# Kernel optimization log

Measured on AMD Instinct MI355X. Metric: run time of the kernel, lower is better.

Reference implementation:

```python
import jax, jax.numpy as jnp
import numpy as np

N = 50000      # nodes
E = 800000     # edges (avg degree 16)
D_IN = 128     # input_dim
H = 64         # hidden_dim (== output_dim)
L = 3          # num_layers


def setup_inputs() -> dict:
    key = jax.random.key(0)
    ks = jax.random.split(key, 24)
    s = 0.05
    p = lambda k, shape: jax.random.normal(k, shape, dtype=jnp.float32) * s
    inp = {}
    inp["node_features"] = jax.random.normal(ks[0], (N, D_IN), dtype=jnp.float32)
    inp["edge_index"] = jax.random.randint(ks[1], (2, E), 0, N, dtype=jnp.int32)
    # pre_mlp: Linear-ReLU-Linear (setup_LRL_nn with hidden_sizes=[hidden_dim])
    inp["pre_w1"] = p(ks[2], (D_IN, H)); inp["pre_b1"] = jnp.zeros((H,), jnp.float32)
    inp["pre_w2"] = p(ks[3], (H, H));    inp["pre_b2"] = jnp.zeros((H,), jnp.float32)
    # learnable skip gates (initialized to ones as in the module)
    inp["skip"] = jnp.ones((L, L), jnp.float32)
    # SAGEConv layers: lin_l (on mean-aggregated neighbors, with bias) + lin_r (root)
    for i in range(L):
        din = H * (i + 1)
        inp[f"wl{i}"] = p(ks[4 + 3 * i], (din, H))
        inp[f"bl{i}"] = jnp.zeros((H,), jnp.float32)
        inp[f"wr{i}"] = p(ks[5 + 3 * i], (din, H))
    # post_mlp: 256->64, 64->64, 64->256, 256->64
    inp["post_w1"] = p(ks[14], (H * (L + 1), H)); inp["post_b1"] = jnp.zeros((H,), jnp.float32)
    inp["post_w2"] = p(ks[15], (H, H));           inp["post_b2"] = jnp.zeros((H,), jnp.float32)
    inp["post_w3"] = p(ks[16], (H, 256));         inp["post_b3"] = jnp.zeros((256,), jnp.float32)
    inp["post_w4"] = p(ks[17], (256, H));         inp["post_b4"] = jnp.zeros((H,), jnp.float32)
    return inp


def _sage(x, src, dst, inv_deg, wl, bl, wr):
    # PyG SAGEConv (mean aggr): lin_l(mean_{j->i} x_j) + lin_r(x_i)
    agg = jax.ops.segment_sum(x[src], dst, num_segments=N) * inv_deg  # [N, Din]
    return agg @ wl + bl + x @ wr


def reference(node_features, edge_index,
              pre_w1, pre_b1, pre_w2, pre_b2, skip,
              wl0, bl0, wr0, wl1, bl1, wr1, wl2, bl2, wr2,
              post_w1, post_b1, post_w2, post_b2, post_w3, post_b3, post_w4, post_b4):
    src, dst = edge_index[0], edge_index[1]
    deg = jax.ops.segment_sum(jnp.ones((E,), jnp.float32), dst, num_segments=N)
    inv_deg = (1.0 / jnp.maximum(deg, 1.0))[:, None]  # [N,1]

    # pre_mlp
    x = jax.nn.relu(node_features @ pre_w1 + pre_b1) @ pre_w2 + pre_b2  # [N,H]

    layers = [(wl0, bl0, wr0), (wl1, bl1, wr1), (wl2, bl2, wr2)]
    all_emb = [x]
    emb = x
    for i, (wl, bl, wr) in enumerate(layers):
        gates = jax.nn.sigmoid(skip[i, :i + 1])  # [i+1]
        curr = jnp.concatenate([all_emb[j] * gates[j] for j in range(i + 1)], axis=1)  # [N, H*(i+1)]
        h = jax.nn.relu(_sage(curr, src, dst, inv_deg, wl, bl, wr))  # [N,H]  (dropout p=0)
        emb = jnp.concatenate([emb, h], axis=1)
        all_emb.append(h)

    s = jnp.sum(emb, axis=-2)  # sums over all nodes -> [H*(L+1)] (faithful to source)
    h = jax.nn.leaky_relu(s @ post_w1 + post_b1, negative_slope=0.1)
    h = jax.nn.relu(h @ post_w2 + post_b2)
    h = jax.nn.relu(h @ post_w3 + post_b3)
    return h @ post_w4 + post_b4  # [H]
```

## Files before the change

### kernel.cpp

```cpp
#include <hip/hip_runtime.h>
#include <math.h>

#define NN 50000
#define NE 800000
#define NB 196

typedef float v4f __attribute__((ext_vector_type(4)));
typedef _Float16 v8h __attribute__((ext_vector_type(8)));


__global__ __launch_bounds__(256) void k_bhist(const int* __restrict__ dst,
                                               int* __restrict__ gbcnt) {
  __shared__ int lcnt[NB];
  int t = threadIdx.x;
  for (int i = t; i < NB; i += 256) lcnt[i] = 0;
  __syncthreads();
  int eb = blockIdx.x * 4096;
#pragma unroll
  for (int i = 0; i < 16; ++i) {
    int e = eb + i * 256 + t;
    if (e < NE) atomicAdd(&lcnt[dst[e] >> 8], 1);
  }
  __syncthreads();
  for (int i = t; i < NB; i += 256)
    if (lcnt[i]) atomicAdd(&gbcnt[i], lcnt[i]);
}

__global__ __launch_bounds__(256) void k_bscan(const int* __restrict__ gbcnt,
                                               int* __restrict__ boff,
                                               int* __restrict__ gcur,
                                               int* __restrict__ offs) {
  __shared__ int sd[256];
  int t = threadIdx.x;
  int v = (t < NB) ? gbcnt[t] : 0;
  sd[t] = v;
  __syncthreads();
  for (int o = 1; o < 256; o <<= 1) {
    int u = (t >= o) ? sd[t - o] : 0;
    __syncthreads();
    sd[t] += u;
    __syncthreads();
  }
  if (t < NB) { int x = sd[t] - v; boff[t] = x; gcur[t] = x; }
  if (t == NB - 1) boff[NB] = sd[t];
  if (t == 0) offs[NN] = NE;
}

__global__ __launch_bounds__(256) void k_bscatter(const int* __restrict__ src,
                                                  const int* __restrict__ dst,
                                                  int* __restrict__ gcur,
                                                  unsigned* __restrict__ ebuf) {
  __shared__ int cnt[NB];
  __shared__ int base[NB];
  int t = threadIdx.x;
  for (int i = t; i < NB; i += 256) cnt[i] = 0;
  __syncthreads();
  int eb = blockIdx.x * 4096;
  unsigned pk[16];
  int bk[16], lp[16];
#pragma unroll
  for (int i = 0; i < 16; ++i) {
    int e = eb + i * 256 + t;
    if (e < NE) {
      int d = dst[e];
      int b = d >> 8;
      pk[i] = ((unsigned)src[e] << 8) | (unsigned)(d & 255);
      bk[i] = b;
      lp[i] = atomicAdd(&cnt[b], 1);
    }
  }
  __syncthreads();
  for (int i = t; i < NB; i += 256)
    base[i] = cnt[i] ? atomicAdd(&gcur[i], cnt[i]) : 0;
  __syncthreads();
#pragma unroll
  for (int i = 0; i < 16; ++i) {
    int e = eb + i * 256 + t;
    if (e < NE) ebuf[base[bk[i]] + lp[i]] = pk[i];
  }
}

__global__ __launch_bounds__(256) void k_bbuild(const unsigned* __restrict__ ebuf,
                                                const int* __restrict__ boff,
                                                int* __restrict__ offs,
                                                float* __restrict__ invd,
                                                int* __restrict__ csr) {
  __shared__ int dcnt[256];
  __shared__ int cur[256];
  int t = threadIdx.x;
  int b = blockIdx.x;
  int node0 = b << 8;
  int es = boff[b], ee = boff[b + 1];
  dcnt[t] = 0;
  __syncthreads();
  for (int e = es + t; e < ee; e += 256) atomicAdd(&dcnt[ebuf[e] & 255], 1);
  __syncthreads();
  int v = dcnt[t];
  cur[t] = v;
  __syncthreads();
  for (int o = 1; o < 256; o <<= 1) {
    int u = (t >= o) ? cur[t - o] : 0;
    __syncthreads();
    cur[t] += u;
    __syncthreads();
  }
  int excl = cur[t] - v;
  int node = node0 + t;
  if (node < NN) {
    offs[node] = es + excl;
    invd[node] = 1.0f / fmaxf((float)v, 1.0f);
  }
  __syncthreads();
  cur[t] = es + excl;
  __syncthreads();
  for (int e = es + t; e < ee; e += 256) {
    unsigned pk = ebuf[e];
    int p = atomicAdd(&cur[pk & 255], 1);
    csr[p] = (int)(pk >> 8);
  }
}

__global__ __launch_bounds__(256) void k_aggregate(
    const _Float16* __restrict__ feat,
    const int* __restrict__ offs, const int* __restrict__ csr,
    const float* __restrict__ invd,
    _Float16* __restrict__ mean, int n) {
  int node = blockIdx.x * 4 + (threadIdx.x >> 6);
  int lane = threadIdx.x & 63;
  int slot = lane >> 3;
  int cg   = lane & 7;
  if (node >= n) return;
  int s = offs[node], e = offs[node + 1];

  float a[8];
#pragma unroll
  for (int i = 0; i < 8; ++i) a[i] = 0.f;

  if (e > s) {
    int emax = e - 1;
    for (int p0 = s; p0 < e; p0 += 16) {
      int pa = p0 + slot, pb = p0 + 8 + slot;
      int ja = __builtin_nontemporal_load(csr + (pa < emax ? pa : emax));
      int jb = __builtin_nontemporal_load(csr + (pb < emax ? pb : emax));
      v8h va = *(const v8h*)(feat + (size_t)ja * 64 + cg * 8);
      v8h vb = *(const v8h*)(feat + (size_t)jb * 64 + cg * 8);
      if (pa < e) {
#pragma unroll
        for (int i = 0; i < 8; ++i) a[i] += (float)va[i];
      }
      if (pb < e) {
#pragma unroll
        for (int i = 0; i < 8; ++i) a[i] += (float)vb[i];
      }
    }
  }
#pragma unroll
  for (int i = 0; i < 8; ++i) {
    a[i] += __shfl_xor(a[i], 8, 64);
    a[i] += __shfl_xor(a[i], 16, 64);
    a[i] += __shfl_xor(a[i], 32, 64);
  }
  if (lane < 8) {
    float d = invd[node];
    v8h o;
#pragma unroll
    for (int i = 0; i < 8; ++i) o[i] = (_Float16)(a[i] * d);
    *(v8h*)(mean + (size_t)node * 64 + lane * 8) = o;
  }
}

struct LinArgs {
  const void*  a[6];
  const float* w[6];
  int gidx[6];
  int stride[6];
  int isf32[6];
  int nsrc;
  const float* bias;
  const float* skip;
  _Float16* outp;
  float* colsum;
  int n;
  int relu;
};

__global__ __launch_bounds__(256) void k_linear(LinArgs A) {
  __shared__ _Float16 sW[2][2][64 * 72];
  const int t    = threadIdx.x;
  const int lane = t & 63;
  const int wv   = t >> 6;
  const int qd   = lane >> 4;
  const int ln   = lane & 15;
  const int n0   = blockIdx.x * 64;

  v4f acc[4];
#pragma unroll
  for (int ct = 0; ct < 4; ++ct) acc[ct] = (v4f){0.f, 0.f, 0.f, 0.f};

  const int sn = t & 63;
  float wreg[16];
  auto loadW = [&](int s) {
    const float* w = A.w[s];
#pragma unroll
    for (int c = 0; c < 2; ++c) {
      int kb = (wv + 4 * c) * 8;
#pragma unroll
      for (int j = 0; j < 8; ++j)
        wreg[c * 8 + j] = w[(size_t)(kb + j) * 64 + sn];
    }
  };
  auto writeW = [&](int s, int b) {
    float gs = 1.0f;
    if (A.gidx[s] >= 0) gs = 1.0f / (1.0f + __expf(-A.skip[A.gidx[s]]));
#pragma unroll
    for (int c = 0; c < 2; ++c) {
      int cb = wv + 4 * c;
      v8h hv, lv;
#pragma unroll
      for (int j = 0; j < 8; ++j) {
        float f = wreg[c * 8 + j] * gs;
        _Float16 h = (_Float16)f;
        hv[j] = h;
        lv[j] = (_Float16)(f - (float)h);
      }
      *(v8h*)(&sW[b][0][sn * 72 + cb * 8]) = hv;
      *(v8h*)(&sW[b][1][sn * 72 + cb * 8]) = lv;
    }
  };

  const int arow = n0 + wv * 16 + ln;
  const bool arv = arow < A.n;
  v8h ah[2];
  auto loadA = [&](int s) {
    if (A.isf32[s]) {
      const float* a = (const float*)A.a[s];
      int st = A.stride[s];
#pragma unroll
      for (int ks = 0; ks < 2; ++ks) {
        v8h hv;
        if (arv) {
          const float* p = a + (size_t)arow * st + ks * 32 + qd * 8;
          float4 u0 = *(const float4*)(p);
          float4 u1 = *(const float4*)(p + 4);
          hv[0] = (_Float16)u0.x; hv[1] = (_Float16)u0.y;
          hv[2] = (_Float16)u0.z; hv[3] = (_Float16)u0.w;
          hv[4] = (_Float16)u1.x; hv[5] = (_Float16)u1.y;
          hv[6] = (_Float16)u1.z; hv[7] = (_Float16)u1.w;
        } else {
#pragma unroll
          for (int j = 0; j < 8; ++j) hv[j] = (_Float16)0.f;
        }
        ah[ks] = hv;
      }
    } else {
      const _Float16* ph = (const _Float16*)A.a[s] + (size_t)arow * 64;
      if (arv) {
#pragma unroll
        for (int ks = 0; ks < 2; ++ks)
          ah[ks] = *(const v8h*)(ph + ks * 32 + qd * 8);
      } else {
        v8h z;
#pragma unroll
        for (int j = 0; j < 8; ++j) z[j] = (_Float16)0.f;
        ah[0] = ah[1] = z;
      }
    }
  };

  loadW(0);
  writeW(0, 0);
  __syncthreads();

  for (int s = 0; s < A.nsrc; ++s) {
    loadA(s);
    if (s + 1 < A.nsrc) loadW(s + 1);
    const _Float16* wh = &sW[s & 1][0][0];
    const _Float16* wl = &sW[s & 1][1][0];
#pragma unroll
    for (int ks = 0; ks < 2; ++ks) {
#pragma unroll
      for (int ct = 0; ct < 4; ++ct) {
        int wn = ct * 16 + ln;
        v8h bh = *(const v8h*)(wh + wn * 72 + ks * 32 + qd * 8);
        v8h bl = *(const v8h*)(wl + wn * 72 + ks * 32 + qd * 8);
        acc[ct] = __builtin_amdgcn_mfma_f32_16x16x32_f16(ah[ks], bh, acc[ct], 0, 0, 0);
        acc[ct] = __builtin_amdgcn_mfma_f32_16x16x32_f16(ah[ks], bl, acc[ct], 0, 0, 0);
      }
    }
    if (s + 1 < A.nsrc) writeW(s + 1, (s + 1) & 1);
    __syncthreads();
  }

  float bvals[4];
#pragma unroll
  for (int ct = 0; ct < 4; ++ct) bvals[ct] = A.bias[ct * 16 + ln];

  float cs[4] = {0.f, 0.f, 0.f, 0.f};
#pragma unroll
  for (int ct = 0; ct < 4; ++ct) {
#pragma unroll
    for (int r = 0; r < 4; ++r) {
      int node = n0 + wv * 16 + qd * 4 + r;
      float v = acc[ct][r] + bvals[ct];
      if (A.relu) v = fmaxf(v, 0.f);
      if (node < A.n) {
        if (A.outp) A.outp[(size_t)node * 64 + ct * 16 + ln] = (_Float16)v;
        cs[ct] += v;
      }
    }
  }
  if (A.colsum) {
    float* red = (float*)&sW[0][0][0];
#pragma unroll
    for (int ct = 0; ct < 4; ++ct) {
      float v = cs[ct];
      v += __shfl_xor(v, 16, 64);
      v += __shfl_xor(v, 32, 64);
      if (qd == 0) red[wv * 64 + ct * 16 + ln] = v;
    }
    __syncthreads();
    if (t < 64) {
      float ssum = red[t] + red[64 + t] + red[128 + t] + red[192 + t];
      atomicAdd(&A.colsum[t], ssum);
    }
  }
}

__global__ __launch_bounds__(256) void k_post(const float* __restrict__ s,
                                              const float* __restrict__ w1, const float* __restrict__ b1,
                                              const float* __restrict__ w2, const float* __restrict__ b2,
                                              const float* __restrict__ w3, const float* __restrict__ b3,
                                              const float* __restrict__ w4, const float* __restrict__ b4,
                                              float* __restrict__ outp) {
  __shared__ float sh[256], h1[64], h2[64], h3[256];
  int t = threadIdx.x;
  sh[t] = s[t];
  __syncthreads();
  if (t < 64) {
    float a = b1[t];
    for (int k = 0; k < 256; ++k) a += sh[k] * w1[k * 64 + t];
    h1[t] = (a >= 0.f) ? a : 0.1f * a;
  }
  __syncthreads();
  if (t < 64) {
    float a = b2[t];
    for (int k = 0; k < 64; ++k) a += h1[k] * w2[k * 64 + t];
    h2[t] = fmaxf(a, 0.f);
  }
  __syncthreads();
  {
    float a = b3[t];
    for (int k = 0; k < 64; ++k) a += h2[k] * w3[k * 256 + t];
    h3[t] = fmaxf(a, 0.f);
  }
  __syncthreads();
  if (t < 64) {
    float a = b4[t];
    for (int k = 0; k < 256; ++k) a += h3[k] * w4[k * 64 + t];
    outp[t] = a;
  }
}

extern "C" void kernel_launch(void* const* d_in, const int* in_sizes, int n_in,
                              void* d_out, int out_size, void* d_ws, size_t ws_size,
                              hipStream_t stream) {
  const float* nf     = (const float*)d_in[0];
  const int*   ei     = (const int*)d_in[1];
  const float* pre_w1 = (const float*)d_in[2];
  const float* pre_b1 = (const float*)d_in[3];
  const float* pre_w2 = (const float*)d_in[4];
  const float* pre_b2 = (const float*)d_in[5];
  const float* skip   = (const float*)d_in[6];
  const float* wl0 = (const float*)d_in[7],  *bl0 = (const float*)d_in[8],  *wr0 = (const float*)d_in[9];
  const float* wl1 = (const float*)d_in[10], *bl1 = (const float*)d_in[11], *wr1 = (const float*)d_in[12];
  const float* wl2 = (const float*)d_in[13], *bl2 = (const float*)d_in[14], *wr2 = (const float*)d_in[15];
  const float* pw1 = (const float*)d_in[16], *pb1 = (const float*)d_in[17];
  const float* pw2 = (const float*)d_in[18], *pb2 = (const float*)d_in[19];
  const float* pw3 = (const float*)d_in[20], *pb3 = (const float*)d_in[21];
  const float* pw4 = (const float*)d_in[22], *pb4 = (const float*)d_in[23];
  float* out = (float*)d_out;

  const int N = NN, E = NE;

  char* ws = (char*)d_ws;
  size_t pos = 0;
  auto alloc = [&](size_t bytes) {
    char* p = ws + pos;
    pos += (bytes + 255) & ~(size_t)255;
    return (void*)p;
  };
  int*      gbcnt = (int*)alloc((size_t)NB * 4);
  int*      boff  = (int*)alloc((size_t)(NB + 1) * 4);
  int*      gcur  = (int*)alloc((size_t)NB * 4);
  unsigned* ebuf  = (unsigned*)alloc((size_t)E * 4);
  int*      offs  = (int*)alloc((size_t)(N + 1) * 4);
  float*    invd  = (float*)alloc((size_t)N * 4);
  int*      csr   = (int*)alloc((size_t)E * 4);
  const size_t PB = (size_t)N * 64 * 2;
  _Float16* t0 = (_Float16*)alloc(PB);
  _Float16* x  = (_Float16*)alloc(PB);
  _Float16* h0 = (_Float16*)alloc(PB);
  _Float16* h1 = (_Float16*)alloc(PB);
  _Float16* m0 = (_Float16*)alloc(PB);
  _Float16* m1 = (_Float16*)alloc(PB);
  _Float16* m2 = (_Float16*)alloc(PB);
  float* sv = (float*)alloc(256 * 4);

  hipMemsetAsync(gbcnt, 0, (size_t)NB * 4, stream);
  hipMemsetAsync(sv, 0, 256 * 4, stream);

  const int* e_src = ei;
  const int* e_dst = ei + E;
  const int EGRID = (E + 4095) / 4096;
  k_bhist<<<EGRID, 256, 0, stream>>>(e_dst, gbcnt);
  k_bscan<<<1, 256, 0, stream>>>(gbcnt, boff, gcur, offs);
  k_bscatter<<<EGRID, 256, 0, stream>>>(e_src, e_dst, gcur, ebuf);
  k_bbuild<<<NB, 256, 0, stream>>>(ebuf, boff, offs, invd, csr);

  const int LGRID = (N + 63) / 64;
  auto lin = [&](int nsrc,
                 const void* a0, int f0, int s0, const float* w0, int g0,
                 const void* a1, int f1, int s1, const float* w1_, int g1,
                 const void* a2, int f2, int s2, const float* w2_, int g2,
                 const void* a3, int f3, int s3, const float* w3_, int g3,
                 const void* a4, int f4, int s4, const float* w4_, int g4,
                 const void* a5, int f5, int s5, const float* w5_, int g5,
                 const float* bias, _Float16* op, float* colsum, int relu) {
    LinArgs A;
    A.a[0] = a0; A.a[1] = a1; A.a[2] = a2; A.a[3] = a3; A.a[4] = a4; A.a[5] = a5;
    A.w[0] = w0; A.w[1] = w1_; A.w[2] = w2_; A.w[3] = w3_; A.w[4] = w4_; A.w[5] = w5_;
    A.gidx[0] = g0; A.gidx[1] = g1; A.gidx[2] = g2; A.gidx[3] = g3; A.gidx[4] = g4; A.gidx[5] = g5;
    A.stride[0] = s0; A.stride[1] = s1; A.stride[2] = s2; A.stride[3] = s3; A.stride[4] = s4; A.stride[5] = s5;
    A.isf32[0] = f0; A.isf32[1] = f1; A.isf32[2] = f2; A.isf32[3] = f3; A.isf32[4] = f4; A.isf32[5] = f5;
    A.nsrc = nsrc; A.bias = bias; A.skip = skip;
    A.outp = op; A.colsum = colsum;
    A.n = N; A.relu = relu;
    k_linear<<<LGRID, 256, 0, stream>>>(A);
  };

  lin(2, nf, 1, 128, pre_w1, -1, nf + 64, 1, 128, pre_w1 + 64 * 64, -1,
      nullptr, 0, 0, nullptr, -1, nullptr, 0, 0, nullptr, -1,
      nullptr, 0, 0, nullptr, -1, nullptr, 0, 0, nullptr, -1,
      pre_b1, t0, nullptr, 1);
  lin(1, t0, 0, 0, pre_w2, -1,
      nullptr, 0, 0, nullptr, -1, nullptr, 0, 0, nullptr, -1,
      nullptr, 0, 0, nullptr, -1, nullptr, 0, 0, nullptr, -1,
      nullptr, 0, 0, nullptr, -1, pre_b2, x, sv, 0);

  k_aggregate<<<(N + 3) / 4, 256, 0, stream>>>(x, offs, csr, invd, m0, N);
  lin(2, m0, 0, 0, wl0, 0, x, 0, 0, wr0, 0,
      nullptr, 0, 0, nullptr, -1, nullptr, 0, 0, nullptr, -1,
      nullptr, 0, 0, nullptr, -1, nullptr, 0, 0, nullptr, -1,
      bl0, h0, sv + 64, 1);

  k_aggregate<<<(N + 3) / 4, 256, 0, stream>>>(h0, offs, csr, invd, m1, N);
  lin(4, m0, 0, 0, wl1, 3, m1, 0, 0, wl1 + 64 * 64, 4,
      x, 0, 0, wr1, 3, h0, 0, 0, wr1 + 64 * 64, 4,
      nullptr, 0, 0, nullptr, -1, nullptr, 0, 0, nullptr, -1,
      bl1, h1, sv + 128, 1);

  k_aggregate<<<(N + 3) / 4, 256, 0, stream>>>(h1, offs, csr, invd, m2, N);
  lin(6, m0, 0, 0, wl2, 6, m1, 0, 0, wl2 + 64 * 64, 7, m2, 0, 0, wl2 + 128 * 64, 8,
      x, 0, 0, wr2, 6, h0, 0, 0, wr2 + 64 * 64, 7, h1, 0, 0, wr2 + 128 * 64, 8,
      bl2, nullptr, sv + 192, 1);

  k_post<<<1, 256, 0, stream>>>(sv, pw1, pb1, pw2, pb2, pw3, pb3, pw4, pb4, out);
}
```

Measured before the change: 365.5 us.

## Gather neighbor features as FP8 and fuse pre-MLP into one kernel

Linear kernels now also write an FP8 (e4m3) copy of each layer's output, staged through shared memory, and the aggregation kernels gather neighbor rows from this 64-byte-per-node buffer instead of fp16 rows. The goal is to halve the bytes moved by the random-access gather, which is the bandwidth-heavy step. The two pre-MLP linears are merged into one kernel that keeps the intermediate tile in LDS, and zeroing of the sum buffer moves into the scan kernel, dropping a launch and a memset. The cost is FP8 quantization error in the aggregated means, which may exceed tolerance.

```diff
diff --git a/kernel.cpp b/kernel.cpp
--- a/kernel.cpp
+++ b/kernel.cpp
@@ -6,7 +6,58 @@
 #define NB 196
 
 typedef float v4f __attribute__((ext_vector_type(4)));
+typedef float v2f __attribute__((ext_vector_type(2)));
 typedef _Float16 v8h __attribute__((ext_vector_type(8)));
+
+__device__ __forceinline__ unsigned char enc8(float v) {
+#if __has_builtin(__builtin_amdgcn_cvt_pk_fp8_f32)
+  return (unsigned char)(__builtin_amdgcn_cvt_pk_fp8_f32(v, v, 0, false) & 0xFF);
+#else
+  unsigned u = __float_as_uint(v);
+  unsigned s = (u >> 24) & 0x80u;
+  unsigned au = u & 0x7fffffffu;
+  float a = __uint_as_float(au);
+  if (au < 0x3C800000u) {
+    int m = (int)(a * 512.0f + 0.5f);
+    if (m >= 8) return (unsigned char)(s | 8u);
+    return (unsigned char)(s | (unsigned)m);
+  }
+  unsigned r = au + 0x7FFFFu + ((au >> 20) & 1u);
+  unsigned e = (r >> 23) - 120u;
+  unsigned man = (r >> 20) & 7u;
+  if (e > 15u) { e = 15u; man = 6u; }
+  return (unsigned char)(s | (e << 3) | man);
+#endif
+}
+
+#if __has_builtin(__builtin_amdgcn_cvt_pk_f32_fp8)
+#define DEC8_HW 1
+#else
+__device__ __forceinline__ float dec8_1(unsigned b) {
+  unsigned s = (b & 0x80u) << 24;
+  unsigned em = b & 0x7fu;
+  float v;
+  if (em >= 8u) v = __uint_as_float((((em >> 3) + 120u) << 23) | ((em & 7u) << 20));
+  else v = (float)em * 0.001953125f;
+  return __uint_as_float(__float_as_uint(v) | s);
+}
+#endif
+
+__device__ __forceinline__ void dec8x8(uint2 u, float* f) {
+#ifdef DEC8_HW
+  v2f p0 = __builtin_amdgcn_cvt_pk_f32_fp8((int)u.x, false);
+  v2f p1 = __builtin_amdgcn_cvt_pk_f32_fp8((int)u.x, true);
+  v2f p2 = __builtin_amdgcn_cvt_pk_f32_fp8((int)u.y, false);
+  v2f p3 = __builtin_amdgcn_cvt_pk_f32_fp8((int)u.y, true);
+  f[0] = p0.x; f[1] = p0.y; f[2] = p1.x; f[3] = p1.y;
+  f[4] = p2.x; f[5] = p2.y; f[6] = p3.x; f[7] = p3.y;
+#else
+#pragma unroll
+  for (int i = 0; i < 4; ++i) f[i] = dec8_1((u.x >> (8 * i)) & 0xFF);
+#pragma unroll
+  for (int i = 0; i < 4; ++i) f[4 + i] = dec8_1((u.y >> (8 * i)) & 0xFF);
+#endif
+}
 
 
 __global__ __launch_bounds__(256) void k_bhist(const int* __restrict__ dst,
@@ -29,9 +80,11 @@
 __global__ __launch_bounds__(256) void k_bscan(const int* __restrict__ gbcnt,
                                                int* __restrict__ boff,
                                                int* __restrict__ gcur,
-                                               int* __restrict__ offs) {
+                                               int* __restrict__ offs,
+                                               float* __restrict__ sv) {
   __shared__ int sd[256];
   int t = threadIdx.x;
+  sv[t] = 0.f;
   int v = (t < NB) ? gbcnt[t] : 0;
   sd[t] = v;
   __syncthreads();
@@ -121,7 +174,7 @@
 }
 
 __global__ __launch_bounds__(256) void k_aggregate(
-    const _Float16* __restrict__ feat,
+    const unsigned char* __restrict__ feat,
     const int* __restrict__ offs, const int* __restrict__ csr,
     const float* __restrict__ invd,
     _Float16* __restrict__ mean, int n) {
@@ -142,15 +195,18 @@
       int pa = p0 + slot, pb = p0 + 8 + slot;
       int ja = __builtin_nontemporal_load(csr + (pa < emax ? pa : emax));
       int jb = __builtin_nontemporal_load(csr + (pb < emax ? pb : emax));
-      v8h va = *(const v8h*)(feat + (size_t)ja * 64 + cg * 8);
-      v8h vb = *(const v8h*)(feat + (size_t)jb * 64 + cg * 8);
+      uint2 ua = *(const uint2*)(feat + (size_t)ja * 64 + cg * 8);
+      uint2 ub = *(const uint2*)(feat + (size_t)jb * 64 + cg * 8);
+      float fa[8], fb[8];
+      dec8x8(ua, fa);
+      dec8x8(ub, fb);
       if (pa < e) {
 #pragma unroll
-        for (int i = 0; i < 8; ++i) a[i] += (float)va[i];
+        for (int i = 0; i < 8; ++i) a[i] += fa[i];
       }
       if (pb < e) {
 #pragma unroll
-        for (int i = 0; i < 8; ++i) a[i] += (float)vb[i];
+        for (int i = 0; i < 8; ++i) a[i] += fb[i];
       }
     }
   }
@@ -170,15 +226,14 @@
 }
 
 struct LinArgs {
-  const void*  a[6];
+  const _Float16* a[6];
   const float* w[6];
   int gidx[6];
-  int stride[6];
-  int isf32[6];
   int nsrc;
   const float* bias;
   const float* skip;
   _Float16* outp;
+  unsigned char* out8;
   float* colsum;
   int n;
   int relu;
@@ -232,38 +287,16 @@
   const bool arv = arow < A.n;
   v8h ah[2];
   auto loadA = [&](int s) {
-    if (A.isf32[s]) {
-      const float* a = (const float*)A.a[s];
-      int st = A.stride[s];
-#pragma unroll
-      for (int ks = 0; ks < 2; ++ks) {
-        v8h hv;
-        if (arv) {
-          const float* p = a + (size_t)arow * st + ks * 32 + qd * 8;
-          float4 u0 = *(const float4*)(p);
-          float4 u1 = *(const float4*)(p + 4);
-          hv[0] = (_Float16)u0.x; hv[1] = (_Float16)u0.y;
-          hv[2] = (_Float16)u0.z; hv[3] = (_Float16)u0.w;
-          hv[4] = (_Float16)u1.x; hv[5] = (_Float16)u1.y;
-          hv[6] = (_Float16)u1.z; hv[7] = (_Float16)u1.w;
-        } else {
-#pragma unroll
-          for (int j = 0; j < 8; ++j) hv[j] = (_Float16)0.f;
-        }
-        ah[ks] = hv;
-      }
+    const _Float16* ph = A.a[s] + (size_t)arow * 64;
+    if (arv) {
+#pragma unroll
+      for (int ks = 0; ks < 2; ++ks)
+        ah[ks] = *(const v8h*)(ph + ks * 32 + qd * 8);
     } else {
-      const _Float16* ph = (const _Float16*)A.a[s] + (size_t)arow * 64;
-      if (arv) {
-#pragma unroll
-        for (int ks = 0; ks < 2; ++ks)
-          ah[ks] = *(const v8h*)(ph + ks * 32 + qd * 8);
-      } else {
-        v8h z;
-#pragma unroll
-        for (int j = 0; j < 8; ++j) z[j] = (_Float16)0.f;
-        ah[0] = ah[1] = z;
-      }
+      v8h z;
+#pragma unroll
+      for (int j = 0; j < 8; ++j) z[j] = (_Float16)0.f;
+      ah[0] = ah[1] = z;
     }
   };
 
@@ -295,22 +328,26 @@
 #pragma unroll
   for (int ct = 0; ct < 4; ++ct) bvals[ct] = A.bias[ct * 16 + ln];
 
+  unsigned char* f8t = (unsigned char*)&sW[1][0][0];
+  float* red = (float*)&sW[0][0][0];
+
   float cs[4] = {0.f, 0.f, 0.f, 0.f};
 #pragma unroll
   for (int ct = 0; ct < 4; ++ct) {
 #pragma unroll
     for (int r = 0; r < 4; ++r) {
-      int node = n0 + wv * 16 + qd * 4 + r;
+      int nb = wv * 16 + qd * 4 + r;
+      int node = n0 + nb;
       float v = acc[ct][r] + bvals[ct];
       if (A.relu) v = fmaxf(v, 0.f);
       if (node < A.n) {
         if (A.outp) A.outp[(size_t)node * 64 + ct * 16 + ln] = (_Float16)v;
+        if (A.out8) f8t[nb * 64 + ct * 16 + ln] = enc8(v);
         cs[ct] += v;
       }
     }
   }
   if (A.colsum) {
-    float* red = (float*)&sW[0][0][0];
 #pragma unroll
     for (int ct = 0; ct < 4; ++ct) {
       float v = cs[ct];
@@ -318,11 +355,181 @@
       v += __shfl_xor(v, 32, 64);
       if (qd == 0) red[wv * 64 + ct * 16 + ln] = v;
     }
-    __syncthreads();
-    if (t < 64) {
-      float ssum = red[t] + red[64 + t] + red[128 + t] + red[192 + t];
-      atomicAdd(&A.colsum[t], ssum);
-    }
+  }
+  if (A.out8 || A.colsum) __syncthreads();
+  if (A.out8) {
+    int row = t >> 2, ch = t & 3;
+    if (n0 + row < A.n) {
+      uint4 val = *(const uint4*)(f8t + row * 64 + ch * 16);
+      *(uint4*)(A.out8 + (size_t)(n0 + row) * 64 + ch * 16) = val;
+    }
+  }
+  if (A.colsum && t < 64) {
+    float ssum = red[t] + red[64 + t] + red[128 + t] + red[192 + t];
+    atomicAdd(&A.colsum[t], ssum);
+  }
+}
+
+__global__ __launch_bounds__(256) void k_pre(
+    const float* __restrict__ nf,
+    const float* __restrict__ w1, const float* __restrict__ b1,
+    const float* __restrict__ w2, const float* __restrict__ b2,
+    _Float16* __restrict__ xout, unsigned char* __restrict__ x8,
+    float* __restrict__ colsum, int n) {
+  __shared__ _Float16 sW[2][2][64 * 72];
+  __shared__ _Float16 atile[64 * 72];
+  const int t    = threadIdx.x;
+  const int lane = t & 63;
+  const int wv   = t >> 6;
+  const int qd   = lane >> 4;
+  const int ln   = lane & 15;
+  const int n0   = blockIdx.x * 64;
+  const int sn   = t & 63;
+
+  float wreg[16];
+  auto loadW = [&](const float* w) {
+#pragma unroll
+    for (int c = 0; c < 2; ++c) {
+      int kb = (wv + 4 * c) * 8;
+#pragma unroll
+      for (int j = 0; j < 8; ++j)
+        wreg[c * 8 + j] = w[(size_t)(kb + j) * 64 + sn];
+    }
+  };
+  auto writeW = [&](int b) {
+#pragma unroll
+    for (int c = 0; c < 2; ++c) {
+      int cb = wv + 4 * c;
+      v8h hv, lv;
+#pragma unroll
+      for (int j = 0; j < 8; ++j) {
+        float f = wreg[c * 8 + j];
+        _Float16 h = (_Float16)f;
+        hv[j] = h;
+        lv[j] = (_Float16)(f - (float)h);
+      }
+      *(v8h*)(&sW[b][0][sn * 72 + cb * 8]) = hv;
+      *(v8h*)(&sW[b][1][sn * 72 + cb * 8]) = lv;
+    }
+  };
+
+  const int arow = n0 + wv * 16 + ln;
+  const bool arv = arow < n;
+  v4f acc[4];
+#pragma unroll
+  for (int ct = 0; ct < 4; ++ct) acc[ct] = (v4f){0.f, 0.f, 0.f, 0.f};
+  v8h ah[2];
+
+  auto loadAf32 = [&](const float* base) {
+#pragma unroll
+    for (int ks = 0; ks < 2; ++ks) {
+      v8h hv;
+      if (arv) {
+        const float* p = base + (size_t)arow * 128 + ks * 32 + qd * 8;
+        float4 u0 = *(const float4*)(p);
+        float4 u1 = *(const float4*)(p + 4);
+        hv[0] = (_Float16)u0.x; hv[1] = (_Float16)u0.y;
+        hv[2] = (_Float16)u0.z; hv[3] = (_Float16)u0.w;
+        hv[4] = (_Float16)u1.x; hv[5] = (_Float16)u1.y;
+        hv[6] = (_Float16)u1.z; hv[7] = (_Float16)u1.w;
+      } else {
+#pragma unroll
+        for (int j = 0; j < 8; ++j) hv[j] = (_Float16)0.f;
+      }
+      ah[ks] = hv;
+    }
+  };
+  auto domfma = [&](int b) {
+    const _Float16* wh = &sW[b][0][0];
+    const _Float16* wl = &sW[b][1][0];
+#pragma unroll
+    for (int ks = 0; ks < 2; ++ks) {
+#pragma unroll
+      for (int ct = 0; ct < 4; ++ct) {
+        int wn = ct * 16 + ln;
+        v8h bh = *(const v8h*)(wh + wn * 72 + ks * 32 + qd * 8);
+        v8h bl = *(const v8h*)(wl + wn * 72 + ks * 32 + qd * 8);
+        acc[ct] = __builtin_amdgcn_mfma_f32_16x16x32_f16(ah[ks], bh, acc[ct], 0, 0, 0);
+        acc[ct] = __builtin_amdgcn_mfma_f32_16x16x32_f16(ah[ks], bl, acc[ct], 0, 0, 0);
+      }
+    }
+  };
+
+  loadW(w1);
+  writeW(0);
+  __syncthreads();
+  loadAf32(nf);
+  loadW(w1 + 64 * 64);
+  domfma(0);
+  writeW(1);
+  __syncthreads();
+  loadAf32(nf + 64);
+  loadW(w2);
+  domfma(1);
+  writeW(0);
+
+  float b1v[4];
+#pragma unroll
+  for (int ct = 0; ct < 4; ++ct) b1v[ct] = b1[ct * 16 + ln];
+#pragma unroll
+  for (int ct = 0; ct < 4; ++ct) {
+#pragma unroll
+    for (int r = 0; r < 4; ++r) {
+      int nb = wv * 16 + qd * 4 + r;
+      float v = fmaxf(acc[ct][r] + b1v[ct], 0.f);
+      atile[nb * 72 + ct * 16 + ln] = (_Float16)v;
+    }
+  }
+#pragma unroll
+  for (int ct = 0; ct < 4; ++ct) acc[ct] = (v4f){0.f, 0.f, 0.f, 0.f};
+  __syncthreads();
+
+  const int trow = wv * 16 + ln;
+#pragma unroll
+  for (int ks = 0; ks < 2; ++ks)
+    ah[ks] = *(const v8h*)(atile + trow * 72 + ks * 32 + qd * 8);
+  domfma(0);
+
+  float b2v[4];
+#pragma unroll
+  for (int ct = 0; ct < 4; ++ct) b2v[ct] = b2[ct * 16 + ln];
+
+  unsigned char* f8t = (unsigned char*)&sW[1][0][0];
+  float* red = (float*)&sW[0][0][0];
+  float cs[4] = {0.f, 0.f, 0.f, 0.f};
+  __syncthreads();
+#pragma unroll
+  for (int ct = 0; ct < 4; ++ct) {
+#pragma unroll
+    for (int r = 0; r < 4; ++r) {
+      int nb = wv * 16 + qd * 4 + r;
+      int node = n0 + nb;
+      float v = acc[ct][r] + b2v[ct];
+      if (node < n) {
+        xout[(size_t)node * 64 + ct * 16 + ln] = (_Float16)v;
+        f8t[nb * 64 + ct * 16 + ln] = enc8(v);
+        cs[ct] += v;
+      }
+    }
+  }
+#pragma unroll
+  for (int ct = 0; ct < 4; ++ct) {
+    float v = cs[ct];
+    v += __shfl_xor(v, 16, 64);
+    v += __shfl_xor(v, 32, 64);
+    if (qd == 0) red[wv * 64 + ct * 16 + ln] = v;
+  }
+  __syncthreads();
+  {
+    int row = t >> 2, ch = t & 3;
+    if (n0 + row < n) {
+      uint4 val = *(const uint4*)(f8t + row * 64 + ch * 16);
+      *(uint4*)(x8 + (size_t)(n0 + row) * 64 + ch * 16) = val;
+    }
+  }
+  if (t < 64) {
+    float ssum = red[t] + red[64 + t] + red[128 + t] + red[192 + t];
+    atomicAdd(&colsum[t], ssum);
   }
 }
 
@@ -397,72 +604,64 @@
   float*    invd  = (float*)alloc((size_t)N * 4);
   int*      csr   = (int*)alloc((size_t)E * 4);
   const size_t PB = (size_t)N * 64 * 2;
-  _Float16* t0 = (_Float16*)alloc(PB);
   _Float16* x  = (_Float16*)alloc(PB);
   _Float16* h0 = (_Float16*)alloc(PB);
   _Float16* h1 = (_Float16*)alloc(PB);
   _Float16* m0 = (_Float16*)alloc(PB);
   _Float16* m1 = (_Float16*)alloc(PB);
   _Float16* m2 = (_Float16*)alloc(PB);
+  unsigned char* f8 = (unsigned char*)alloc((size_t)N * 64);
   float* sv = (float*)alloc(256 * 4);
 
   hipMemsetAsync(gbcnt, 0, (size_t)NB * 4, stream);
-  hipMemsetAsync(sv, 0, 256 * 4, stream);
 
   const int* e_src = ei;
   const int* e_dst = ei + E;
   const int EGRID = (E + 4095) / 4096;
   k_bhist<<<EGRID, 256, 0, stream>>>(e_dst, gbcnt);
-  k_bscan<<<1, 256, 0, stream>>>(gbcnt, boff, gcur, offs);
+  k_bscan<<<1, 256, 0, stream>>>(gbcnt, boff, gcur, offs, sv);
   k_bscatter<<<EGRID, 256, 0, stream>>>(e_src, e_dst, gcur, ebuf);
   k_bbuild<<<NB, 256, 0, stream>>>(ebuf, boff, offs, invd, csr);
 
   const int LGRID = (N + 63) / 64;
   auto lin = [&](int nsrc,
-                 const void* a0, int f0, int s0, const float* w0, int g0,
-                 const void* a1, int f1, int s1, const float* w1_, int g1,
-                 const void* a2, int f2, int s2, const float* w2_, int g2,
-                 const void* a3, int f3, int s3, const float* w3_, int g3,
-                 const void* a4, int f4, int s4, const float* w4_, int g4,
-                 const void* a5, int f5, int s5, const float* w5_, int g5,
-                 const float* bias, _Float16* op, float* colsum, int relu) {
+                 const _Float16* a0, const float* w0, int g0,
+                 const _Float16* a1, const float* w1_, int g1,
+                 const _Float16* a2, const float* w2_, int g2,
+                 const _Float16* a3, const float* w3_, int g3,
+                 const _Float16* a4, const float* w4_, int g4,
+                 const _Float16* a5, const float* w5_, int g5,
+                 const float* bias, _Float16* op, unsigned char* o8,
+                 float* colsum, int relu) {
     LinArgs A;
     A.a[0] = a0; A.a[1] = a1; A.a[2] = a2; A.a[3] = a3; A.a[4] = a4; A.a[5] = a5;
     A.w[0] = w0; A.w[1] = w1_; A.w[2] = w2_; A.w[3] = w3_; A.w[4] = w4_; A.w[5] = w5_;
     A.gidx[0] = g0; A.gidx[1] = g1; A.gidx[2] = g2; A.gidx[3] = g3; A.gidx[4] = g4; A.gidx[5] = g5;
-    A.stride[0] = s0; A.stride[1] = s1; A.stride[2] = s2; A.stride[3] = s3; A.stride[4] = s4; A.stride[5] = s5;
-    A.isf32[0] = f0; A.isf32[1] = f1; A.isf32[2] = f2; A.isf32[3] = f3; A.isf32[4] = f4; A.isf32[5] = f5;
     A.nsrc = nsrc; A.bias = bias; A.skip = skip;
-    A.outp = op; A.colsum = colsum;
+    A.outp = op; A.out8 = o8; A.colsum = colsum;
     A.n = N; A.relu = relu;
     k_linear<<<LGRID, 256, 0, stream>>>(A);
   };
 
-  lin(2, nf, 1, 128, pre_w1, -1, nf + 64, 1, 128, pre_w1 + 64 * 64, -1,
-      nullptr, 0, 0, nullptr, -1, nullptr, 0, 0, nullptr, -1,
-      nullptr, 0, 0, nullptr, -1, nullptr, 0, 0, nullptr, -1,
-      pre_b1, t0, nullptr, 1);
-  lin(1, t0, 0, 0, pre_w2, -1,
-      nullptr, 0, 0, nullptr, -1, nullptr, 0, 0, nullptr, -1,
-      nullptr, 0, 0, nullptr, -1, nullptr, 0, 0, nullptr, -1,
-      nullptr, 0, 0, nullptr, -1, pre_b2, x, sv, 0);
-
-  k_aggregate<<<(N + 3) / 4, 256, 0, stream>>>(x, offs, csr, invd, m0, N);
-  lin(2, m0, 0, 0, wl0, 0, x, 0, 0, wr0, 0,
-      nullptr, 0, 0, nullptr, -1, nullptr, 0, 0, nullptr, -1,
-      nullptr, 0, 0, nullptr, -1, nullptr, 0, 0, nullptr, -1,
-      bl0, h0, sv + 64, 1);
-
-  k_aggregate<<<(N + 3) / 4, 256, 0, stream>>>(h0, offs, csr, invd, m1, N);
-  lin(4, m0, 0, 0, wl1, 3, m1, 0, 0, wl1 + 64 * 64, 4,
-      x, 0, 0, wr1, 3, h0, 0, 0, wr1 + 64 * 64, 4,
-      nullptr, 0, 0, nullptr, -1, nullptr, 0, 0, nullptr, -1,
-      bl1, h1, sv + 128, 1);
-
-  k_aggregate<<<(N + 3) / 4, 256, 0, stream>>>(h1, offs, csr, invd, m2, N);
-  lin(6, m0, 0, 0, wl2, 6, m1, 0, 0, wl2 + 64 * 64, 7, m2, 0, 0, wl2 + 128 * 64, 8,
-      x, 0, 0, wr2, 6, h0, 0, 0, wr2 + 64 * 64, 7, h1, 0, 0, wr2 + 128 * 64, 8,
-      bl2, nullptr, sv + 192, 1);
+  k_pre<<<LGRID, 256, 0, stream>>>(nf, pre_w1, pre_b1, pre_w2, pre_b2,
+                                   x, f8, sv, N);
+
+  k_aggregate<<<(N + 3) / 4, 256, 0, stream>>>(f8, offs, csr, invd, m0, N);
+  lin(2, m0, wl0, 0, x, wr0, 0,
+      nullptr, nullptr, -1, nullptr, nullptr, -1,
+      nullptr, nullptr, -1, nullptr, nullptr, -1,
+      bl0, h0, f8, sv + 64, 1);
+
+  k_aggregate<<<(N + 3) / 4, 256, 0, stream>>>(f8, offs, csr, invd, m1, N);
+  lin(4, m0, wl1, 3, m1, wl1 + 64 * 64, 4,
+      x, wr1, 3, h0, wr1 + 64 * 64, 4,
+      nullptr, nullptr, -1, nullptr, nullptr, -1,
+      bl1, h1, f8, sv + 128, 1);
+
+  k_aggregate<<<(N + 3) / 4, 256, 0, stream>>>(f8, offs, csr, invd, m2, N);
+  lin(6, m0, wl2, 6, m1, wl2 + 64 * 64, 7, m2, wl2 + 128 * 64, 8,
+      x, wr2, 6, h0, wr2 + 64 * 64, 7, h1, wr2 + 128 * 64, 8,
+      bl2, nullptr, nullptr, sv + 192, 1);
 
   k_post<<<1, 256, 0, stream>>>(sv, pw1, pb1, pw2, pb2, pw3, pb3, pw4, pb4, out);
 }
```

Result: faster. 356.6 us (-2.4%).
